# Kernel tuning notes

Hardware: AMD Instinct MI355X
Metric: run time of the kernel (lower is better)

The kernel has to match this reference:

```python
import jax, jax.numpy as jnp
import numpy as np

B, T, A, C = 8, 512, 512, 8
D, NHEAD, FF, L = 256, 8, 1024, 3
DEC_FF = 512
V = 32          # categorical cardinality per feature (tables have 1+V rows, row 0 = padding)
NEG = -1e9      # finite stand-in for -inf: exp underflows to 0 exactly, masked rows are zeroed anyway


def layer_norm(x, g, b, eps=1e-5):
    m = jnp.mean(x, axis=-1, keepdims=True)
    v = jnp.mean(jnp.square(x - m), axis=-1, keepdims=True)
    return (x - m) * jax.lax.rsqrt(v + eps) * g + b


def mha(q_in, k_in, v_in, wq, wk, wv, wo, nhead, mask=None):
    b, _, dm = q_in.shape
    dh = dm // nhead
    # faithful to the original torch code: .view(B, nhead, -1, d_head) with NO transpose
    q = (q_in @ wq).reshape(b, nhead, -1, dh)
    k = (k_in @ wk).reshape(b, nhead, -1, dh)
    v = (v_in @ wv).reshape(b, nhead, -1, dh)
    u = jnp.einsum('bhqd,bhkd->bhqk', q, k) / float(np.sqrt(dh))
    if mask is not None:
        m = mask[:, None]  # [B,1,q,k] (broadcast)
        attn = jax.nn.softmax(jnp.where(m, NEG, u), axis=-1)
        attn = jnp.where(m, 0.0, attn)
    else:
        attn = jax.nn.softmax(u, axis=-1)
    return jnp.einsum('bhqk,bhkd->bhqd', attn, v).reshape(b, -1, dm) @ wo


def embed(x, tables, wo, bo):
    # all features categorical: Embedder sums per-feature embeddings of (1 + x), then a Linear
    nf = x.shape[-1]
    e = tables[jnp.arange(nf), 1 + x]  # [B,N,nf,D]
    return jnp.sum(e, axis=2) @ wo + bo


def encoder(x, mask, wq, wk, wv, wo, w1, b1, w2, b2, g1, be1, g2, be2):
    for i in range(wq.shape[0]):
        x = layer_norm(x + mha(x, x, x, wq[i], wk[i], wv[i], wo[i], NHEAD, mask), g1[i], be1[i])
        x = layer_norm(x + jax.nn.relu(x @ w1[i] + b1[i]) @ w2[i] + b2[i], g2[i], be2[i])
    return x


def forward(tasks, agents, indices, P):
    (emb_t, emb_t_wo, emb_t_bo, emb_a, emb_a_wo, emb_a_bo,
     et_wq, et_wk, et_wv, et_wo, et_w1, et_b1, et_w2, et_b2, et_g1, et_be1, et_g2, et_be2,
     ea_wq, ea_wk, ea_wv, ea_wo, ea_w1, ea_b1, ea_w2, ea_b2, ea_g1, ea_be1, ea_g2, ea_be2,
     de_wq, de_wk, de_wv, de_wo, de_w1, de_b1, de_w2, de_b2, de_g1, de_be1, de_g2, de_be2,
     do_wq, do_wk) = P
    padding_mask = jnp.all(tasks == -1, axis=-1)[:, None, :]  # [B,1,T]
    # _get_mask: scatter assigned task indices (slot 0 absorbs the -1 padding)
    b_idx = jnp.arange(B)[:, None, None]
    a_idx = jnp.arange(A)[None, :, None]
    am = jnp.zeros((B, A, 1 + T), jnp.bool_).at[b_idx, a_idx, 1 + indices].set(True)
    assignment_mask = jnp.any(am[..., 1:], axis=1, keepdims=True)      # [B,1,T]
    full_mask = jnp.all(indices != -1, axis=-1, keepdims=True)         # [B,A,1]
    mask = jnp.swapaxes(assignment_mask | padding_mask | full_mask, -1, -2)  # [B,T,A]
    ht = encoder(embed(tasks, emb_t, emb_t_wo, emb_t_bo), padding_mask,
                 et_wq, et_wk, et_wv, et_wo, et_w1, et_b1, et_w2, et_b2, et_g1, et_be1, et_g2, et_be2)
    ha = encoder(embed(agents, emb_a, emb_a_wo, emb_a_bo), padding_mask,
                 ea_wq, ea_wk, ea_wv, ea_wo, ea_w1, ea_b1, ea_w2, ea_b2, ea_g1, ea_be1, ea_g2, ea_be2)
    # decoder (x=ha, h=ht): queries are the task stream, keys/values the agent stream
    h = layer_norm(ht + mha(ht, ha, ha, de_wq, de_wk, de_wv, de_wo, NHEAD, mask), de_g1, de_be1)
    h = layer_norm(h + jax.nn.relu(h @ de_w1 + de_b1) @ de_w2 + de_b2, de_g2, de_be2)
    # output attention (nhead=1, d_head=D); mean over the singleton head dim is identity
    scores = jnp.einsum('btd,bad->bta', h @ do_wq, ha @ do_wk) / float(np.sqrt(D))
    probs = 8.0 * jnp.tanh(scores)                                     # [B,T,A]
    p = jax.nn.softmax(jnp.where(mask, NEG, probs), axis=-1)
    p = jnp.where(mask, 0.0, p)
    return jnp.swapaxes(p, -1, -2)                                     # [B,A,T]


def setup_inputs():
    key = jax.random.key(0)
    kc = iter(jax.random.split(key, 64))
    def w(*shape):
        return jax.random.normal(next(kc), shape, jnp.float32) * 0.05
    def table(nf):
        t = jax.random.normal(next(kc), (nf, 1 + V, D), jnp.float32) * 0.05
        return t.at[:, 0].set(0.0)  # padding_idx=0
    inp = {
        'tasks': jax.random.randint(next(kc), (B, T, 4), 0, V, jnp.int32),
        'agents': jax.random.randint(next(kc), (B, A, 2), 0, V, jnp.int32),
        'indices': jax.random.randint(next(kc), (B, A, C), 0, T + 1, jnp.int32) - 1,  # in [-1, T-1]
        'emb_t': table(4), 'emb_t_wo': w(D, D), 'emb_t_bo': jnp.zeros((D,), jnp.float32),
        'emb_a': table(2), 'emb_a_wo': w(D, D), 'emb_a_bo': jnp.zeros((D,), jnp.float32),
    }
    for pre in ('et', 'ea'):
        inp[pre + '_wq'] = w(L, D, D); inp[pre + '_wk'] = w(L, D, D)
        inp[pre + '_wv'] = w(L, D, D); inp[pre + '_wo'] = w(L, D, D)
        inp[pre + '_w1'] = w(L, D, FF); inp[pre + '_b1'] = jnp.zeros((L, FF), jnp.float32)
        inp[pre + '_w2'] = w(L, FF, D); inp[pre + '_b2'] = jnp.zeros((L, D), jnp.float32)
        inp[pre + '_g1'] = jnp.ones((L, D), jnp.float32); inp[pre + '_be1'] = jnp.zeros((L, D), jnp.float32)
        inp[pre + '_g2'] = jnp.ones((L, D), jnp.float32); inp[pre + '_be2'] = jnp.zeros((L, D), jnp.float32)
    inp['de_wq'] = w(D, D); inp['de_wk'] = w(D, D); inp['de_wv'] = w(D, D); inp['de_wo'] = w(D, D)
    inp['de_w1'] = w(D, DEC_FF); inp['de_b1'] = jnp.zeros((DEC_FF,), jnp.float32)
    inp['de_w2'] = w(DEC_FF, D); inp['de_b2'] = jnp.zeros((D,), jnp.float32)
    inp['de_g1'] = jnp.ones((D,), jnp.float32); inp['de_be1'] = jnp.zeros((D,), jnp.float32)
    inp['de_g2'] = jnp.ones((D,), jnp.float32); inp['de_be2'] = jnp.zeros((D,), jnp.float32)
    inp['do_wq'] = w(D, D); inp['do_wk'] = w(D, D)
    return inp


def reference(tasks, agents, indices, emb_t, emb_t_wo, emb_t_bo, emb_a, emb_a_wo, emb_a_bo,
              et_wq, et_wk, et_wv, et_wo, et_w1, et_b1, et_w2, et_b2, et_g1, et_be1, et_g2, et_be2,
              ea_wq, ea_wk, ea_wv, ea_wo, ea_w1, ea_b1, ea_w2, ea_b2, ea_g1, ea_be1, ea_g2, ea_be2,
              de_wq, de_wk, de_wv, de_wo, de_w1, de_b1, de_w2, de_b2, de_g1, de_be1, de_g2, de_be2,
              do_wq, do_wk):
    P = (emb_t, emb_t_wo, emb_t_bo, emb_a, emb_a_wo, emb_a_bo,
         et_wq, et_wk, et_wv, et_wo, et_w1, et_b1, et_w2, et_b2, et_g1, et_be1, et_g2, et_be2,
         ea_wq, ea_wk, ea_wv, ea_wo, ea_w1, ea_b1, ea_w2, ea_b2, ea_g1, ea_be1, ea_g2, ea_be2,
         de_wq, de_wk, de_wv, de_wo, de_w1, de_b1, de_w2, de_b2, de_g1, de_be1, de_g2, de_be2,
         do_wq, do_wk)
    return forward(tasks, agents, indices, P)
```

## Files before the change

### kernel.cpp

```cpp
#include <hip/hip_runtime.h>
#include <hip/hip_bf16.h>

constexpr int CB = 8;
constexpr int CT = 512;
constexpr int CA = 512;
constexpr int CC = 8;
constexpr int CD = 256;
constexpr float NEGV = -1.0e9f;

typedef __attribute__((ext_vector_type(8))) short bf16x8;
typedef __attribute__((ext_vector_type(4))) float f32x4;

__device__ inline short f2bf(float f) {
  uint32_t u = __float_as_uint(f);
  uint32_t r = (u + 0x7FFFu + ((u >> 16) & 1u)) >> 16;
  return (short)r;
}

__global__ void mask_prep_kernel(const int* __restrict__ tasks,
                                 const int* __restrict__ indices,
                                 int* __restrict__ asgn, int* __restrict__ fullm,
                                 int* __restrict__ padm) {
  int i = blockIdx.x * blockDim.x + threadIdx.x;
  if (i >= CB * CT) return;
  asgn[i] = 0;
  const int* tp = tasks + i * 4;
  padm[i] = (tp[0] == -1) && (tp[1] == -1) && (tp[2] == -1) && (tp[3] == -1);
  const int* ip = indices + i * CC;
  int full = 1;
#pragma unroll
  for (int c = 0; c < CC; ++c) full &= (ip[c] != -1);
  fullm[i] = full;
}

__global__ void mask_assign_kernel(const int* __restrict__ indices, int* __restrict__ asgn) {
  int i = blockIdx.x * blockDim.x + threadIdx.x;
  if (i >= CB * CA * CC) return;
  int b = i / (CA * CC);
  int idx = indices[i];
  if (idx >= 0) asgn[b * CT + idx] = 1;
}

struct TDesc { const float* src; short* dst; int K; int N; int tbase; };
struct TArgs { TDesc d[46]; int nd; };

__global__ __launch_bounds__(256) void trans_kernel(TArgs a) {
  __shared__ short Ts[64][72];
  const int bid = blockIdx.x;
  int w = 0;
#pragma unroll 1
  for (int i = 1; i < a.nd; ++i)
    if (a.d[i].tbase <= bid) w = i;
  const TDesc de = a.d[w];
  const int ti = bid - de.tbase;
  const int ntn = de.N >> 6;
  const int n0 = (ti % ntn) * 64, k0 = (ti / ntn) * 64;
  const int t = threadIdx.x;
  const int kk = t >> 4, c4 = (t & 15) * 4;
#pragma unroll
  for (int r = 0; r < 4; ++r) {
    float4 v = *(const float4*)(de.src + (size_t)(k0 + kk + r * 16) * de.N + n0 + c4);
    Ts[c4 + 0][kk + r * 16] = f2bf(v.x);
    Ts[c4 + 1][kk + r * 16] = f2bf(v.y);
    Ts[c4 + 2][kk + r * 16] = f2bf(v.z);
    Ts[c4 + 3][kk + r * 16] = f2bf(v.w);
  }
  __syncthreads();
  const int n = t >> 3, k8 = (t & 7) * 8;
#pragma unroll
  for (int r = 0; r < 2; ++r)
    *(bf16x8*)(de.dst + (size_t)(n0 + n + r * 32) * de.K + k0 + k8) =
        *(bf16x8*)&Ts[n + r * 32][k8];
}

__global__ void embed2_kernel(const int* __restrict__ tasks, const int* __restrict__ agents,
                              const float* __restrict__ tab_t, const float* __restrict__ tab_a,
                              short* __restrict__ out) {
  int row = blockIdx.x;
  int lane = threadIdx.x;
  const int* tp;
  const float* table;
  int nf;
  short* dst;
  if (row < 4096) {
    tp = tasks + row * 4; table = tab_t; nf = 4; dst = out + (size_t)row * CD;
  } else {
    int r = row - 4096;
    tp = agents + r * 2; table = tab_a; nf = 2; dst = out + 1048576 + (size_t)r * CD;
  }
  float4 acc = make_float4(0.f, 0.f, 0.f, 0.f);
  for (int f = 0; f < nf; ++f) {
    int t = 1 + tp[f];
    float4 v = *(const float4*)(table + ((size_t)f * 33 + t) * CD + lane * 4);
    acc.x += v.x; acc.y += v.y; acc.z += v.z; acc.w += v.w;
  }
  short4 o;
  o.x = f2bf(acc.x); o.y = f2bf(acc.y); o.z = f2bf(acc.z); o.w = f2bf(acc.w);
  *(short4*)(dst + lane * 4) = o;
}

__device__ __forceinline__ void ln_row(float* x, const float* res, const float* g,
                                       const float* b, short* xb, int row, int lane) {
  float4 xv = *(const float4*)(x + (size_t)row * CD + lane * 4);
  float4 rv = *(const float4*)(res + (size_t)row * CD + lane * 4);
  float v0 = xv.x + rv.x, v1 = xv.y + rv.y, v2 = xv.z + rv.z, v3 = xv.w + rv.w;
  float s = v0 + v1 + v2 + v3;
  float s2 = v0 * v0 + v1 * v1 + v2 * v2 + v3 * v3;
#pragma unroll
  for (int off = 32; off >= 1; off >>= 1) {
    s += __shfl_xor(s, off);
    s2 += __shfl_xor(s2, off);
  }
  float mean = s * (1.0f / CD);
  float var = s2 * (1.0f / CD) - mean * mean;
  float rstd = rsqrtf(var + 1e-5f);
  float4 gv = *(const float4*)(g + lane * 4);
  float4 bv = *(const float4*)(b + lane * 4);
  float4 o;
  o.x = (v0 - mean) * rstd * gv.x + bv.x;
  o.y = (v1 - mean) * rstd * gv.y + bv.y;
  o.z = (v2 - mean) * rstd * gv.z + bv.z;
  o.w = (v3 - mean) * rstd * gv.w + bv.w;
  *(float4*)(x + (size_t)row * CD + lane * 4) = o;
  short4 ob;
  ob.x = f2bf(o.x); ob.y = f2bf(o.y); ob.z = f2bf(o.z); ob.w = f2bf(o.w);
  *(short4*)(xb + (size_t)row * CD + lane * 4) = ob;
}

__global__ __launch_bounds__(256) void ln_add1_kernel(
    float* __restrict__ x, const float* __restrict__ res,
    const float* __restrict__ g, const float* __restrict__ b, short* __restrict__ xb) {
  int row = blockIdx.x * 4 + (threadIdx.x >> 6);
  ln_row(x, res, g, b, xb, row, threadIdx.x & 63);
}

__global__ __launch_bounds__(256) void ln_add2_kernel(
    float* __restrict__ x0, const float* __restrict__ r0, const float* __restrict__ g0,
    const float* __restrict__ b0, short* __restrict__ s0,
    float* __restrict__ x1, const float* __restrict__ r1, const float* __restrict__ g1,
    const float* __restrict__ b1, short* __restrict__ s1) {
  int row = blockIdx.x * 4 + (threadIdx.x >> 6);
  int lane = threadIdx.x & 63;
  if (row < 4096) ln_row(x0, r0, g0, b0, s0, row, lane);
  else ln_row(x1, r1, g1, b1, s1, row - 4096, lane);
}

template <int CMODE, bool BIAS, bool RELU>
__device__ __forceinline__ void gemm_body(
    const short* __restrict__ Ab, const short* __restrict__ Bb,
    const float* __restrict__ bias, float* __restrict__ Cf, short* __restrict__ Cbf,
    int Ndim, int Kdim, int bm, int bn) {
  __shared__ short As[128][72];
  __shared__ short Bs[64][72];
  const int t = threadIdx.x;
  const int lane = t & 63, wave = t >> 6;
  const int wm = wave * 32;
  const int fr = lane & 15, fs = lane >> 4;
  const int srow = t >> 3, sk8 = (t & 7) * 8;

  f32x4 acc[2][4] = {};

  for (int k0 = 0; k0 < Kdim; k0 += 64) {
#pragma unroll
    for (int r = 0; r < 4; ++r)
      *(bf16x8*)&As[srow + r * 32][sk8] =
          *(const bf16x8*)(Ab + (size_t)(bm + srow + r * 32) * Kdim + k0 + sk8);
#pragma unroll
    for (int r = 0; r < 2; ++r)
      *(bf16x8*)&Bs[srow + r * 32][sk8] =
          *(const bf16x8*)(Bb + (size_t)(bn + srow + r * 32) * Kdim + k0 + sk8);
    __syncthreads();
#pragma unroll
    for (int kk = 0; kk < 2; ++kk) {
      bf16x8 a0 = *(bf16x8*)&As[wm + fr][kk * 32 + fs * 8];
      bf16x8 a1 = *(bf16x8*)&As[wm + 16 + fr][kk * 32 + fs * 8];
      bf16x8 bf0 = *(bf16x8*)&Bs[fr][kk * 32 + fs * 8];
      bf16x8 bf1 = *(bf16x8*)&Bs[16 + fr][kk * 32 + fs * 8];
      bf16x8 bf2 = *(bf16x8*)&Bs[32 + fr][kk * 32 + fs * 8];
      bf16x8 bf3 = *(bf16x8*)&Bs[48 + fr][kk * 32 + fs * 8];
      acc[0][0] = __builtin_amdgcn_mfma_f32_16x16x32_bf16(a0, bf0, acc[0][0], 0, 0, 0);
      acc[0][1] = __builtin_amdgcn_mfma_f32_16x16x32_bf16(a0, bf1, acc[0][1], 0, 0, 0);
      acc[0][2] = __builtin_amdgcn_mfma_f32_16x16x32_bf16(a0, bf2, acc[0][2], 0, 0, 0);
      acc[0][3] = __builtin_amdgcn_mfma_f32_16x16x32_bf16(a0, bf3, acc[0][3], 0, 0, 0);
      acc[1][0] = __builtin_amdgcn_mfma_f32_16x16x32_bf16(a1, bf0, acc[1][0], 0, 0, 0);
      acc[1][1] = __builtin_amdgcn_mfma_f32_16x16x32_bf16(a1, bf1, acc[1][1], 0, 0, 0);
      acc[1][2] = __builtin_amdgcn_mfma_f32_16x16x32_bf16(a1, bf2, acc[1][2], 0, 0, 0);
      acc[1][3] = __builtin_amdgcn_mfma_f32_16x16x32_bf16(a1, bf3, acc[1][3], 0, 0, 0);
    }
    __syncthreads();
  }

#pragma unroll
  for (int fi = 0; fi < 2; ++fi)
#pragma unroll
    for (int fj = 0; fj < 4; ++fj) {
      int row0 = bm + wm + fi * 16 + fs * 4;
      int col = bn + fj * 16 + fr;
      float bv = BIAS ? bias[col] : 0.0f;
#pragma unroll
      for (int r = 0; r < 4; ++r) {
        float v = acc[fi][fj][r] + bv;
        if (RELU) v = fmaxf(v, 0.0f);
        if (CMODE == 0 || CMODE == 2) Cf[(size_t)(row0 + r) * Ndim + col] = v;
        if (CMODE == 1 || CMODE == 2) Cbf[(size_t)(row0 + r) * Ndim + col] = f2bf(v);
      }
    }
}

struct GArgs {
  const short* A[8];
  const short* Bm[8];
  const float* bias[8];
  float* Cf[8];
  short* Cb[8];
  int Ndim, Kdim;
};

template <int CMODE, bool BIAS, bool RELU>
__global__ __launch_bounds__(256) void mgemm_kernel(GArgs ga) {
  int z = blockIdx.z;
  gemm_body<CMODE, BIAS, RELU>(ga.A[z], ga.Bm[z], ga.bias[z], ga.Cf[z], ga.Cb[z],
                               ga.Ndim, ga.Kdim, blockIdx.x * 128, blockIdx.y * 64);
}

template <int MODE>
__global__ __launch_bounds__(512) void mattn_kernel(
    const short* __restrict__ qb, const short* __restrict__ kb, const short* __restrict__ vb,
    short* __restrict__ ob,
    const int* __restrict__ asgn, const int* __restrict__ fullm, const int* __restrict__ padm) {
  __shared__ short Ks[512][40];
  __shared__ short Vt[32][520];
  __shared__ short Pb[8][16][40];
  __shared__ unsigned int mwords[16];
  const int bh = blockIdx.x;
  const int b = (bh >> 3) & 7;
  const size_t base = (size_t)bh * (512 * 32);
  const int tid = threadIdx.x;

#pragma unroll
  for (int r = 0; r < 4; ++r) {
    int i = r * 512 + tid;
    int row = i >> 2, seg = (i & 3) * 8;
    *(bf16x8*)&Ks[row][seg] = *(const bf16x8*)(kb + base + row * 32 + seg);
  }
  {
    int d = tid & 31, g = tid >> 5;
#pragma unroll
    for (int r = 0; r < 8; ++r) {
      int key0 = (r * 16 + g) * 4;
      const short* vp = vb + base + (size_t)key0 * 32 + d;
      unsigned short p0 = (unsigned short)vp[0];
      unsigned short p1 = (unsigned short)vp[32];
      unsigned short p2 = (unsigned short)vp[64];
      unsigned short p3 = (unsigned short)vp[96];
      int lo = ((int)p0) | (((int)p1) << 16);
      int hi = ((int)p2) | (((int)p3) << 16);
      *(int2*)&Vt[d][key0] = make_int2(lo, hi);
    }
  }
  if (tid < 16) {
    unsigned w = 0;
    for (int tl = 0; tl < 32; ++tl) {
      int key = tl * 16 + tid;
      int m = (MODE == 0) ? padm[b * CT + key] : fullm[b * CA + key];
      w |= ((unsigned)(m != 0)) << tl;
    }
    mwords[tid] = w;
  }
  __syncthreads();

  const int wave = tid >> 6, lane = tid & 63;
  const int fr = lane & 15, fs = lane >> 4;
  const int q0 = blockIdx.y * 128 + wave * 16;
  const int q = q0 + fr;

  bf16x8 qf = *(const bf16x8*)(qb + base + (size_t)q * 32 + fs * 8);

  unsigned qmbits = 0;
  if (MODE == 1) {
    int qm = asgn[b * CT + q] | padm[b * CT + q];
    qmbits = qm ? 0xFFFFFFFFu : 0u;
  }
  unsigned mw[4];
#pragma unroll
  for (int g = 0; g < 4; ++g) mw[g] = mwords[4 * fs + g] | qmbits;

  f32x4 s[32];
#pragma unroll
  for (int tl = 0; tl < 32; ++tl) {
    bf16x8 kf = *(bf16x8*)&Ks[tl * 16 + fr][fs * 8];
    f32x4 z = {0.f, 0.f, 0.f, 0.f};
    s[tl] = __builtin_amdgcn_mfma_f32_16x16x32_bf16(kf, qf, z, 0, 0, 0);
  }
  const float sc = 0.17677669529663687f;
  float mx = -3.0e38f;
#pragma unroll
  for (int tl = 0; tl < 32; ++tl)
#pragma unroll
    for (int g = 0; g < 4; ++g) mx = fmaxf(mx, s[tl][g]);
  mx = fmaxf(mx, __shfl_xor(mx, 16));
  mx = fmaxf(mx, __shfl_xor(mx, 32));
  float sum = 0.f;
#pragma unroll
  for (int tl = 0; tl < 32; ++tl)
#pragma unroll
    for (int g = 0; g < 4; ++g) {
      float e = __expf((s[tl][g] - mx) * sc);
      e = ((mw[g] >> tl) & 1u) ? 0.0f : e;
      s[tl][g] = e;
      sum += e;
    }
  sum += __shfl_xor(sum, 16);
  sum += __shfl_xor(sum, 32);
  float inv = (sum > 0.f) ? (1.0f / sum) : 0.0f;

  f32x4 o0 = {0.f, 0.f, 0.f, 0.f}, o1 = {0.f, 0.f, 0.f, 0.f};
#pragma unroll
  for (int c = 0; c < 16; ++c) {
    int w0, w1, w2, w3;
    asm("v_cvt_pk_bf16_f32 %0, %1, %2" : "=v"(w0) : "v"(s[2 * c][0]), "v"(s[2 * c][1]));
    asm("v_cvt_pk_bf16_f32 %0, %1, %2" : "=v"(w1) : "v"(s[2 * c][2]), "v"(s[2 * c][3]));
    asm("v_cvt_pk_bf16_f32 %0, %1, %2" : "=v"(w2) : "v"(s[2 * c + 1][0]), "v"(s[2 * c + 1][1]));
    asm("v_cvt_pk_bf16_f32 %0, %1, %2" : "=v"(w3) : "v"(s[2 * c + 1][2]), "v"(s[2 * c + 1][3]));
    *(int2*)&Pb[wave][fr][4 * fs] = make_int2(w0, w1);
    *(int2*)&Pb[wave][fr][16 + 4 * fs] = make_int2(w2, w3);
    asm volatile("s_waitcnt lgkmcnt(0)" ::: "memory");
    __builtin_amdgcn_sched_barrier(0);
    bf16x8 af = *(bf16x8*)&Pb[wave][fr][8 * fs];
    bf16x8 v0 = *(bf16x8*)&Vt[fr][32 * c + 8 * fs];
    bf16x8 v1 = *(bf16x8*)&Vt[16 + fr][32 * c + 8 * fs];
    o0 = __builtin_amdgcn_mfma_f32_16x16x32_bf16(af, v0, o0, 0, 0, 0);
    o1 = __builtin_amdgcn_mfma_f32_16x16x32_bf16(af, v1, o1, 0, 0, 0);
  }
#pragma unroll
  for (int g = 0; g < 4; ++g) {
    float iv = __shfl(inv, fs * 4 + g);
    int qq = q0 + fs * 4 + g;
    ob[base + (size_t)qq * 32 + fr] = f2bf(o0[g] * iv);
    ob[base + (size_t)qq * 32 + 16 + fr] = f2bf(o1[g] * iv);
  }
}

__global__ void final_kernel(const float* __restrict__ scores,
                             const int* __restrict__ asgn, const int* __restrict__ fullm,
                             const int* __restrict__ padm, float* __restrict__ out) {
  int row = blockIdx.x;
  int b = row >> 9, t = row & 511;
  int lane = threadIdx.x;
  int qm = asgn[row] | padm[row];
  const float* sp = scores + (size_t)row * 512;
  float v[8];
  int mk[8];
#pragma unroll
  for (int m = 0; m < 8; ++m) {
    int a = lane + (m << 6);
    float val = 8.0f * tanhf(sp[a] * (1.0f / 16.0f));
    int masked = qm | fullm[b * CA + a];
    mk[m] = masked;
    v[m] = masked ? NEGV : val;
  }
  float mx = v[0];
#pragma unroll
  for (int m = 1; m < 8; ++m) mx = fmaxf(mx, v[m]);
#pragma unroll
  for (int off = 32; off >= 1; off >>= 1) mx = fmaxf(mx, __shfl_xor(mx, off));
  float sum = 0.f, e[8];
#pragma unroll
  for (int m = 0; m < 8; ++m) { e[m] = __expf(v[m] - mx); sum += e[m]; }
#pragma unroll
  for (int off = 32; off >= 1; off >>= 1) sum += __shfl_xor(sum, off);
  float inv = 1.0f / sum;
#pragma unroll
  for (int m = 0; m < 8; ++m) {
    int a = lane + (m << 6);
    float p = mk[m] ? 0.0f : e[m] * inv;
    out[(size_t)b * (CA * CT) + (size_t)a * CT + t] = p;
  }
}

extern "C" void kernel_launch(void* const* d_in, const int* in_sizes, int n_in,
                              void* d_out, int out_size, void* d_ws, size_t ws_size,
                              hipStream_t stream) {
  const int* tasks = (const int*)d_in[0];
  const int* agents = (const int*)d_in[1];
  const int* indices = (const int*)d_in[2];
  const float* emb_t = (const float*)d_in[3];
  const float* emb_t_wo = (const float*)d_in[4];
  const float* emb_t_bo = (const float*)d_in[5];
  const float* emb_a = (const float*)d_in[6];
  const float* emb_a_wo = (const float*)d_in[7];
  const float* emb_a_bo = (const float*)d_in[8];
  const float* de_wq = (const float*)d_in[33];
  const float* de_wk = (const float*)d_in[34];
  const float* de_wv = (const float*)d_in[35];
  const float* de_wo = (const float*)d_in[36];
  const float* de_w1 = (const float*)d_in[37];
  const float* de_b1 = (const float*)d_in[38];
  const float* de_w2 = (const float*)d_in[39];
  const float* de_b2 = (const float*)d_in[40];
  const float* de_g1 = (const float*)d_in[41];
  const float* de_be1 = (const float*)d_in[42];
  const float* de_g2 = (const float*)d_in[43];
  const float* de_be2 = (const float*)d_in[44];
  const float* do_wq = (const float*)d_in[45];
  const float* do_wk = (const float*)d_in[46];

  float* ws = (float*)d_ws;
  float* ht = ws + 0;
  float* ha = ws + 1048576;
  short* htb = (short*)(ws + 2097152);
  short* hab = (short*)(ws + 2621440);
  short* qall = (short*)(ws + 3145728);
  short* kall = (short*)(ws + 4194304);
  short* vall = (short*)(ws + 5242880);
  short* t1b = (short*)(ws + 6291456);
  float* scores = ws + 6291456;
  float* t2 = ws + 10485760;
  short* wT = (short*)(ws + 12582912);
  int* asgn = (int*)(ws + 15400000);
  int* fullm = asgn + 4096;
  int* padm = asgn + 8192;

  TArgs ta;
  int idx = 0, tb = 0;
  size_t doff = 0;
  short* Wp[46];
  auto addw = [&](const float* s, int K, int N) {
    Wp[idx] = wT + doff;
    ta.d[idx] = {s, wT + doff, K, N, tb};
    tb += (K >> 6) * (N >> 6);
    doff += (size_t)K * N;
    ++idx;
  };
  addw(emb_t_wo, 256, 256);
  addw(emb_a_wo, 256, 256);
  for (int enc = 0; enc < 2; ++enc) {
    int pb = enc ? 21 : 9;
    const float* wq = (const float*)d_in[pb + 0];
    const float* wk = (const float*)d_in[pb + 1];
    const float* wv = (const float*)d_in[pb + 2];
    const float* wo = (const float*)d_in[pb + 3];
    const float* w1 = (const float*)d_in[pb + 4];
    const float* w2 = (const float*)d_in[pb + 6];
    for (int l = 0; l < 3; ++l) {
      addw(wq + l * 65536, 256, 256);
      addw(wk + l * 65536, 256, 256);
      addw(wv + l * 65536, 256, 256);
      addw(wo + l * 65536, 256, 256);
    }
    for (int l = 0; l < 3; ++l) addw(w1 + l * 262144, 256, 1024);
    for (int l = 0; l < 3; ++l) addw(w2 + l * 262144, 1024, 256);
  }
  addw(de_wq, 256, 256);
  addw(de_wk, 256, 256);
  addw(de_wv, 256, 256);
  addw(de_wo, 256, 256);
  addw(de_w1, 256, 512);
  addw(de_w2, 512, 256);
  addw(do_wq, 256, 256);
  addw(do_wk, 256, 256);
  ta.nd = idx;

  mask_prep_kernel<<<16, 256, 0, stream>>>(tasks, indices, asgn, fullm, padm);
  mask_assign_kernel<<<128, 256, 0, stream>>>(indices, asgn);
  trans_kernel<<<tb, 256, 0, stream>>>(ta);

  GArgs ga{};

  embed2_kernel<<<8192, 64, 0, stream>>>(tasks, agents, emb_t, emb_a, t1b);
  ga.A[0] = t1b;            ga.Bm[0] = Wp[0]; ga.bias[0] = emb_t_bo; ga.Cf[0] = ht; ga.Cb[0] = htb;
  ga.A[1] = t1b + 1048576;  ga.Bm[1] = Wp[1]; ga.bias[1] = emb_a_bo; ga.Cf[1] = ha; ga.Cb[1] = hab;
  ga.Ndim = 256; ga.Kdim = 256;
  mgemm_kernel<2, true, false><<<dim3(32, 4, 2), 256, 0, stream>>>(ga);

  const float* b1t = (const float*)d_in[14];
  const float* b2t = (const float*)d_in[16];
  const float* g1t = (const float*)d_in[17];
  const float* be1t = (const float*)d_in[18];
  const float* g2t = (const float*)d_in[19];
  const float* be2t = (const float*)d_in[20];
  const float* b1a = (const float*)d_in[26];
  const float* b2a = (const float*)d_in[28];
  const float* g1a = (const float*)d_in[29];
  const float* be1a = (const float*)d_in[30];
  const float* g2a = (const float*)d_in[31];
  const float* be2a = (const float*)d_in[32];

  for (int l = 0; l < 3; ++l) {
    for (int j = 0; j < 3; ++j) {
      ga.A[j] = htb;     ga.Bm[j] = Wp[2 + l * 4 + j];
      ga.A[3 + j] = hab; ga.Bm[3 + j] = Wp[20 + l * 4 + j];
    }
    short* outs[6] = {qall, kall, vall, qall + 1048576, kall + 1048576, vall + 1048576};
    for (int j = 0; j < 6; ++j) ga.Cb[j] = outs[j];
    ga.Ndim = 256; ga.Kdim = 256;
    mgemm_kernel<1, false, false><<<dim3(32, 4, 6), 256, 0, stream>>>(ga);
    mattn_kernel<0><<<dim3(128, 4, 1), 512, 0, stream>>>(qall, kall, vall, t1b,
                                                         asgn, fullm, padm);
    ga.A[0] = t1b;           ga.Bm[0] = Wp[2 + l * 4 + 3];  ga.Cf[0] = t2;
    ga.A[1] = t1b + 1048576; ga.Bm[1] = Wp[20 + l * 4 + 3]; ga.Cf[1] = t2 + 1048576;
    ga.Ndim = 256; ga.Kdim = 256;
    mgemm_kernel<0, false, false><<<dim3(32, 4, 2), 256, 0, stream>>>(ga);
    ln_add2_kernel<<<2048, 256, 0, stream>>>(ht, t2, g1t + l * 256, be1t + l * 256, htb,
                                             ha, t2 + 1048576, g1a + l * 256, be1a + l * 256, hab);
    ga.A[0] = htb; ga.Bm[0] = Wp[14 + l]; ga.bias[0] = b1t + l * 1024; ga.Cb[0] = t1b;
    ga.A[1] = hab; ga.Bm[1] = Wp[32 + l]; ga.bias[1] = b1a + l * 1024; ga.Cb[1] = t1b + 4194304;
    ga.Ndim = 1024; ga.Kdim = 256;
    mgemm_kernel<1, true, true><<<dim3(32, 16, 2), 256, 0, stream>>>(ga);
    ga.A[0] = t1b;           ga.Bm[0] = Wp[17 + l]; ga.bias[0] = b2t + l * 256; ga.Cf[0] = t2;
    ga.A[1] = t1b + 4194304; ga.Bm[1] = Wp[35 + l]; ga.bias[1] = b2a + l * 256; ga.Cf[1] = t2 + 1048576;
    ga.Ndim = 256; ga.Kdim = 1024;
    mgemm_kernel<0, true, false><<<dim3(32, 4, 2), 256, 0, stream>>>(ga);
    ln_add2_kernel<<<2048, 256, 0, stream>>>(ht, t2, g2t + l * 256, be2t + l * 256, htb,
                                             ha, t2 + 1048576, g2a + l * 256, be2a + l * 256, hab);
  }

  ga.A[0] = htb; ga.Bm[0] = Wp[38]; ga.Cb[0] = qall;
  ga.A[1] = hab; ga.Bm[1] = Wp[39]; ga.Cb[1] = kall;
  ga.A[2] = hab; ga.Bm[2] = Wp[40]; ga.Cb[2] = vall;
  ga.Ndim = 256; ga.Kdim = 256;
  mgemm_kernel<1, false, false><<<dim3(32, 4, 3), 256, 0, stream>>>(ga);
  mattn_kernel<1><<<dim3(64, 4, 1), 512, 0, stream>>>(qall, kall, vall, t1b,
                                                      asgn, fullm, padm);
  ga.A[0] = t1b; ga.Bm[0] = Wp[41]; ga.Cf[0] = t2;
  ga.Ndim = 256; ga.Kdim = 256;
  mgemm_kernel<0, false, false><<<dim3(32, 4, 1), 256, 0, stream>>>(ga);
  ln_add1_kernel<<<1024, 256, 0, stream>>>(ht, t2, de_g1, de_be1, htb);
  ga.A[0] = htb; ga.Bm[0] = Wp[42]; ga.bias[0] = de_b1; ga.Cb[0] = t1b;
  ga.Ndim = 512; ga.Kdim = 256;
  mgemm_kernel<1, true, true><<<dim3(32, 8, 1), 256, 0, stream>>>(ga);
  ga.A[0] = t1b; ga.Bm[0] = Wp[43]; ga.bias[0] = de_b2; ga.Cf[0] = t2;
  ga.Ndim = 256; ga.Kdim = 512;
  mgemm_kernel<0, true, false><<<dim3(32, 4, 1), 256, 0, stream>>>(ga);
  ln_add1_kernel<<<1024, 256, 0, stream>>>(ht, t2, de_g2, de_be2, htb);

  ga.A[0] = htb; ga.Bm[0] = Wp[44]; ga.Cb[0] = qall;
  ga.A[1] = hab; ga.Bm[1] = Wp[45]; ga.Cb[1] = kall;
  ga.Ndim = 256; ga.Kdim = 256;
  mgemm_kernel<1, false, false><<<dim3(32, 4, 2), 256, 0, stream>>>(ga);
  for (int b = 0; b < 8; ++b) {
    ga.A[b] = qall + (size_t)b * 131072;
    ga.Bm[b] = kall + (size_t)b * 131072;
    ga.Cf[b] = scores + (size_t)b * 262144;
  }
  ga.Ndim = 512; ga.Kdim = 256;
  mgemm_kernel<0, false, false><<<dim3(4, 8, 8), 256, 0, stream>>>(ga);
  final_kernel<<<4096, 64, 0, stream>>>(scores, asgn, fullm, padm, (float*)d_out);
}
```

Measured before the change: 487.7 us.

## Double-buffer GEMM tiles with direct global-to-LDS loads and XOR swizzle

Replaces the register-staged global-to-shared copy in the GEMM body with async global_load_lds into two LDS buffers, so the next K tile is prefetched while the current one is consumed by MFMA. The padded shared layout becomes an unpadded one with an XOR column swizzle to avoid bank conflicts. The goal is to hide global memory latency and drop one barrier per iteration. LDS use doubles, which may reduce occupancy, and the single barrier per step depends on the async load ordering being correct.

```diff
diff --git a/kernel.cpp b/kernel.cpp
--- a/kernel.cpp
+++ b/kernel.cpp
@@ -150,34 +150,57 @@
     const short* __restrict__ Ab, const short* __restrict__ Bb,
     const float* __restrict__ bias, float* __restrict__ Cf, short* __restrict__ Cbf,
     int Ndim, int Kdim, int bm, int bn) {
-  __shared__ short As[128][72];
-  __shared__ short Bs[64][72];
+  __shared__ __align__(16) short As[2][128 * 64];
+  __shared__ __align__(16) short Bs[2][64 * 64];
   const int t = threadIdx.x;
   const int lane = t & 63, wave = t >> 6;
   const int wm = wave * 32;
   const int fr = lane & 15, fs = lane >> 4;
-  const int srow = t >> 3, sk8 = (t & 7) * 8;
+  const int fr7 = fr & 7;
+
+  const int srow = t >> 3;
+  const int lc = (t & 7) ^ (srow & 7);
+  const short* Asrc = Ab + (size_t)(bm + srow) * Kdim + lc * 8;
+  const short* Bsrc = Bb + (size_t)(bn + srow) * Kdim + lc * 8;
 
   f32x4 acc[2][4] = {};
 
+  auto stage = [&](int buf, int k0) {
+#pragma unroll
+    for (int r = 0; r < 4; ++r)
+      __builtin_amdgcn_global_load_lds(
+          (const __attribute__((address_space(1))) void*)(Asrc + (size_t)(r * 32) * Kdim + k0),
+          (__attribute__((address_space(3))) void*)(&As[buf][r * 2048 + wave * 512]),
+          16, 0, 0);
+#pragma unroll
+    for (int r = 0; r < 2; ++r)
+      __builtin_amdgcn_global_load_lds(
+          (const __attribute__((address_space(1))) void*)(Bsrc + (size_t)(r * 32) * Kdim + k0),
+          (__attribute__((address_space(3))) void*)(&Bs[buf][r * 2048 + wave * 512]),
+          16, 0, 0);
+  };
+
+  stage(0, 0);
+  __syncthreads();
+  int buf = 0;
+#pragma unroll 1
   for (int k0 = 0; k0 < Kdim; k0 += 64) {
-#pragma unroll
-    for (int r = 0; r < 4; ++r)
-      *(bf16x8*)&As[srow + r * 32][sk8] =
-          *(const bf16x8*)(Ab + (size_t)(bm + srow + r * 32) * Kdim + k0 + sk8);
-#pragma unroll
-    for (int r = 0; r < 2; ++r)
-      *(bf16x8*)&Bs[srow + r * 32][sk8] =
-          *(const bf16x8*)(Bb + (size_t)(bn + srow + r * 32) * Kdim + k0 + sk8);
-    __syncthreads();
+    if (k0 + 64 < Kdim) stage(buf ^ 1, k0 + 64);
+    const short* A0 = &As[buf][(wm + fr) * 64];
+    const short* A1 = &As[buf][(wm + 16 + fr) * 64];
+    const short* B0 = &Bs[buf][fr * 64];
+    const short* B1 = &Bs[buf][(16 + fr) * 64];
+    const short* B2 = &Bs[buf][(32 + fr) * 64];
+    const short* B3 = &Bs[buf][(48 + fr) * 64];
 #pragma unroll
     for (int kk = 0; kk < 2; ++kk) {
-      bf16x8 a0 = *(bf16x8*)&As[wm + fr][kk * 32 + fs * 8];
-      bf16x8 a1 = *(bf16x8*)&As[wm + 16 + fr][kk * 32 + fs * 8];
-      bf16x8 bf0 = *(bf16x8*)&Bs[fr][kk * 32 + fs * 8];
-      bf16x8 bf1 = *(bf16x8*)&Bs[16 + fr][kk * 32 + fs * 8];
-      bf16x8 bf2 = *(bf16x8*)&Bs[32 + fr][kk * 32 + fs * 8];
-      bf16x8 bf3 = *(bf16x8*)&Bs[48 + fr][kk * 32 + fs * 8];
+      const int co = (((kk * 4) + fs) ^ fr7) * 8;
+      bf16x8 a0 = *(bf16x8*)(A0 + co);
+      bf16x8 a1 = *(bf16x8*)(A1 + co);
+      bf16x8 bf0 = *(bf16x8*)(B0 + co);
+      bf16x8 bf1 = *(bf16x8*)(B1 + co);
+      bf16x8 bf2 = *(bf16x8*)(B2 + co);
+      bf16x8 bf3 = *(bf16x8*)(B3 + co);
       acc[0][0] = __builtin_amdgcn_mfma_f32_16x16x32_bf16(a0, bf0, acc[0][0], 0, 0, 0);
       acc[0][1] = __builtin_amdgcn_mfma_f32_16x16x32_bf16(a0, bf1, acc[0][1], 0, 0, 0);
       acc[0][2] = __builtin_amdgcn_mfma_f32_16x16x32_bf16(a0, bf2, acc[0][2], 0, 0, 0);
@@ -188,6 +211,7 @@
       acc[1][3] = __builtin_amdgcn_mfma_f32_16x16x32_bf16(a1, bf3, acc[1][3], 0, 0, 0);
     }
     __syncthreads();
+    buf ^= 1;
   }
 
 #pragma unroll
```

New measurement: 483.2 us. About the same (-0.9%).
